# Kernel tuning notes

Hardware: AMD Instinct MI355X
Metric: run time of the kernel (lower is better)

The kernel has to match this reference:

```python
import jax, jax.numpy as jnp
import numpy as np

LN_EPS = 1e-5

def _ln(x, g, b):
    # LayerNorm over last dim; torch normalized_shape=[1,H] on [B,1,H] reduces to this
    mu = jnp.mean(x, axis=-1, keepdims=True)
    var = jnp.var(x, axis=-1, keepdims=True)
    return (x - mu) * jax.lax.rsqrt(var + LN_EPS) * g + b


def setup_inputs() -> dict:
    key = jax.random.key(0)
    B, T, D, H = 32, 2048, 512, 128
    ks = jax.random.split(key, 10)
    stdu = 1.0 / np.sqrt(H)
    u = lambda k, sh: jax.random.uniform(k, sh, jnp.float32, -stdu, stdu)
    return {
        "x": jax.random.normal(ks[0], (B, T, D), jnp.float32),
        "W_f": u(ks[1], (D, H)), "W_i": u(ks[2], (D, H)),
        "W_o": u(ks[3], (D, H)), "W_c": u(ks[4], (D, H)),
        "U_f": u(ks[5], (H, H)), "U_i": u(ks[6], (H, H)),
        "U_o": u(ks[7], (H, H)), "U_c": u(ks[8], (H, H)),
        "b_f": jnp.ones((H,), jnp.float32),
        "b_i": jnp.zeros((H,), jnp.float32),
        "b_o": jnp.zeros((H,), jnp.float32),
        "b_c": jnp.zeros((H,), jnp.float32),
        "ln_f_g": jnp.ones((H,), jnp.float32), "ln_f_b": jnp.zeros((H,), jnp.float32),
        "ln_i_g": jnp.ones((H,), jnp.float32), "ln_i_b": jnp.zeros((H,), jnp.float32),
        "ln_o_g": jnp.ones((H,), jnp.float32), "ln_o_b": jnp.zeros((H,), jnp.float32),
        "ln_c_g": jnp.ones((H,), jnp.float32), "ln_c_b": jnp.zeros((H,), jnp.float32),
        "h0": jnp.zeros((B, H), jnp.float32),
        "c0": jnp.zeros((B, H), jnp.float32),
        "zoneout_mask": jax.random.randint(ks[9], (T,), 0, 2, jnp.int32),
    }


def reference(x, W_f, W_i, W_o, W_c, U_f, U_i, U_o, U_c,
              b_f, b_i, b_o, b_c,
              ln_f_g, ln_f_b, ln_i_g, ln_i_b, ln_o_g, ln_o_b, ln_c_g, ln_c_b,
              h0, c0, zoneout_mask):
    xs = jnp.swapaxes(x, 0, 1)                       # [T, B, D]
    m = zoneout_mask.astype(x.dtype)[:, None, None]  # [T, 1, 1] zoneout indicator

    def step(carry, inp):
        h, c = carry
        x_t, mt = inp
        f = jax.nn.sigmoid(_ln(x_t @ W_f + h @ U_f + b_f, ln_f_g, ln_f_b))
        i = jax.nn.sigmoid(_ln(x_t @ W_i + h @ U_i + b_i, ln_i_g, ln_i_b))
        o = jax.nn.sigmoid(_ln(x_t @ W_o + h @ U_o + b_o, ln_o_g, ln_o_b))
        ch = jax.nn.sigmoid(_ln(x_t @ W_c + h @ U_c + b_c, ln_c_g, ln_c_b))
        c_new = mt * c + (1.0 - mt) * (f * c + i * ch)
        # NOTE: source applies sigmoid (not tanh) to the cell state
        h_new = mt * h + (1.0 - mt) * (o * jax.nn.sigmoid(c_new))
        return (h_new, c_new), h_new

    (h_T, c_T), out_seq = jax.lax.scan(step, (h0, c0), (xs, m))
    return jnp.swapaxes(out_seq, 0, 1), h_T          # [B, T, H], [B, H]
```

## Files before the change

### kernel.cpp

```cpp
#include <hip/hip_runtime.h>
#include <hip/hip_bf16.h>

#define Bx 32
#define Tt 2048
#define Dd 512
#define Hh 128

typedef __attribute__((ext_vector_type(8))) short short8;
typedef __attribute__((ext_vector_type(4))) float f32x4;

static __device__ __forceinline__ short f2bf(float f) {
    __hip_bfloat16 h = __float2bfloat16(f);
    return *reinterpret_cast<short*>(&h);
}
static __device__ __forceinline__ float sigm(float x) {
    return 1.f / (1.f + __expf(-x));
}

template<int CTRL>
static __device__ __forceinline__ float dpp_add(float v) {
    return v + __int_as_float(__builtin_amdgcn_update_dpp(
        0, __float_as_int(v), CTRL, 0xF, 0xF, true));
}
static __device__ __forceinline__ float swz_xor16_add(float v) {
    return v + __int_as_float(__builtin_amdgcn_ds_swizzle(__float_as_int(v), 0x401F));
}

#define BARRIER_LGKM() asm volatile("s_waitcnt lgkmcnt(0)\n\ts_barrier" ::: "memory")

__global__ __launch_bounds__(512, 2) void gemm_xw_mfma(
    const float* __restrict__ X,
    const float* __restrict__ W0, const float* __restrict__ W1,
    const float* __restrict__ W2, const float* __restrict__ W3,
    float* __restrict__ G)
{
    __shared__ __align__(16) short As[128][40];
    __shared__ __align__(16) short Bs[512][40];

    const int tid  = threadIdx.x;
    const int m0   = blockIdx.x * 128;
    const int lane = tid & 63;
    const int w    = tid >> 6;
    const int wr   = w >> 2, wc = w & 3;
    const int l15  = lane & 15, kb = lane >> 4;

    const int bn   = tid;
    const int gate = bn >> 7;
    const int j    = bn & 127;
    const float* __restrict__ Wg = (gate == 0) ? W0 : (gate == 1) ? W1 : (gate == 2) ? W2 : W3;

    const int am = tid >> 2;
    const int ak = (tid & 3) * 8;

    f32x4 acc[4][8];
    #pragma unroll
    for (int mt = 0; mt < 4; ++mt)
        #pragma unroll
        for (int nt = 0; nt < 8; ++nt)
            acc[mt][nt] = (f32x4){0.f, 0.f, 0.f, 0.f};

    for (int k0 = 0; k0 < Dd; k0 += 32) {
        {
            const float4* xp = (const float4*)&X[(size_t)(m0 + am) * Dd + k0 + ak];
            float4 v0 = xp[0], v1 = xp[1];
            short8 s;
            s[0] = f2bf(v0.x); s[1] = f2bf(v0.y); s[2] = f2bf(v0.z); s[3] = f2bf(v0.w);
            s[4] = f2bf(v1.x); s[5] = f2bf(v1.y); s[6] = f2bf(v1.z); s[7] = f2bf(v1.w);
            *(short8*)&As[am][ak] = s;
        }
        #pragma unroll
        for (int rc = 0; rc < 4; ++rc) {
            float v[8];
            #pragma unroll
            for (int r = 0; r < 8; ++r)
                v[r] = Wg[(size_t)(k0 + rc * 8 + r) * Hh + j];
            short8 s;
            #pragma unroll
            for (int r = 0; r < 8; ++r) s[r] = f2bf(v[r]);
            *(short8*)&Bs[bn][rc * 8] = s;
        }
        __syncthreads();

        short8 a[4], b[8];
        #pragma unroll
        for (int mt = 0; mt < 4; ++mt)
            a[mt] = *(const short8*)&As[wr * 64 + mt * 16 + l15][kb * 8];
        #pragma unroll
        for (int nt = 0; nt < 8; ++nt)
            b[nt] = *(const short8*)&Bs[wc * 128 + nt * 16 + l15][kb * 8];
        #pragma unroll
        for (int mt = 0; mt < 4; ++mt)
            #pragma unroll
            for (int nt = 0; nt < 8; ++nt)
                acc[mt][nt] = __builtin_amdgcn_mfma_f32_16x16x32_bf16(a[mt], b[nt], acc[mt][nt], 0, 0, 0);
        __syncthreads();
    }

    #pragma unroll
    for (int mt = 0; mt < 4; ++mt)
        #pragma unroll
        for (int nt = 0; nt < 8; ++nt)
            #pragma unroll
            for (int r = 0; r < 4; ++r)
                G[(size_t)(m0 + wr * 64 + mt * 16 + kb * 4 + r) * 512 + wc * 128 + nt * 16 + l15]
                    = acc[mt][nt][r];
}

__global__ __launch_bounds__(512, 1) void lstm_scan_mfma(
    const float* __restrict__ G,
    const float* __restrict__ Uf, const float* __restrict__ Ui,
    const float* __restrict__ Uo, const float* __restrict__ Uc,
    const float* __restrict__ bf_, const float* __restrict__ bi_,
    const float* __restrict__ bo_, const float* __restrict__ bc_,
    const float* __restrict__ lnfg, const float* __restrict__ lnfb,
    const float* __restrict__ lnig, const float* __restrict__ lnib,
    const float* __restrict__ lnog, const float* __restrict__ lnob,
    const float* __restrict__ lncg, const float* __restrict__ lncb,
    const float* __restrict__ h0, const float* __restrict__ c0,
    const int* __restrict__ zmask,
    float* __restrict__ out, float* __restrict__ hT)
{
    const int tid  = threadIdx.x;
    const int lane = tid & 63;
    const int w    = tid >> 6;
    const int b0   = blockIdx.x * 4;

    __shared__ __align__(16) short Ap[16 * 136];
    __shared__ __align__(16) float ST[512 * 10];
    __shared__ unsigned short act[Tt];
    __shared__ int wsum[8], wpre[8];
    __shared__ int nact_sh;

    const int gate = w >> 1;
    const float* __restrict__ Ug = (gate == 0) ? Uf : (gate == 1) ? Ui : (gate == 2) ? Uo : Uc;
    const int n0  = w * 64;
    const int l15 = lane & 15;
    const int kb  = lane >> 4;

    short8 bfr[4][4];
    #pragma unroll
    for (int nt = 0; nt < 4; ++nt) {
        const int jloc = (n0 & 127) + nt * 16 + l15;
        #pragma unroll
        for (int ks = 0; ks < 4; ++ks) {
            short8 v;
            #pragma unroll
            for (int r = 0; r < 8; ++r) {
                const int krow = ks * 32 + kb * 8 + r;
                v[r] = f2bf(Ug[krow * Hh + jloc]);
            }
            bfr[nt][ks] = v;
        }
    }

    const int rowL = tid >> 5;
    const int bL   = rowL >> 2;
    const int gL   = rowL & 3;
    const int cl   = tid & 31;
    const float* lnGp = (gL == 0) ? lnfg : (gL == 1) ? lnig : (gL == 2) ? lnog : lncg;
    const float* lnBp = (gL == 0) ? lnfb : (gL == 1) ? lnib : (gL == 2) ? lnob : lncb;
    const float* bgp  = (gL == 0) ? bf_  : (gL == 1) ? bi_  : (gL == 2) ? bo_  : bc_;
    float lgam[4], lbet[4], lbias[4];
    #pragma unroll
    for (int kk = 0; kk < 4; ++kk) {
        const int jc = cl + 32 * kk;
        lgam[kk] = lnGp[jc]; lbet[kk] = lnBp[jc]; lbias[kk] = bgp[jc];
    }

    const int ob = tid >> 7;
    const int oj = tid & 127;
    float hval = h0[(b0 + ob) * Hh + oj];
    float cval = c0[(b0 + ob) * Hh + oj];

    for (int i = tid; i < 16 * 136; i += 512) Ap[i] = 0;
    int* zst = (int*)ST;
    for (int t = tid; t < Tt; t += 512) zst[t] = zmask[t];
    __syncthreads();

    Ap[ob * 136 + oj] = f2bf(hval);

    {
        const int base_t = tid * 4;
        const int f0 = (zst[base_t] == 0), f1 = (zst[base_t + 1] == 0);
        const int f2 = (zst[base_t + 2] == 0), f3 = (zst[base_t + 3] == 0);
        const int cnt = f0 + f1 + f2 + f3;
        int scan = cnt;
        #pragma unroll
        for (int off = 1; off <= 32; off <<= 1) {
            int v = __shfl_up(scan, off);
            if (lane >= off) scan += v;
        }
        if (lane == 63) wsum[w] = scan;
        __syncthreads();
        if (tid == 0) {
            int s = 0;
            #pragma unroll
            for (int i = 0; i < 8; ++i) { wpre[i] = s; s += wsum[i]; }
            nact_sh = s;
        }
        __syncthreads();
        int pos = wpre[w] + scan - cnt;
        if (f0) act[pos++] = (unsigned short)(base_t);
        if (f1) act[pos++] = (unsigned short)(base_t + 1);
        if (f2) act[pos++] = (unsigned short)(base_t + 2);
        if (f3) act[pos++] = (unsigned short)(base_t + 3);
    }
    __syncthreads();
    const int nact = nact_sh;

    const int firstA = (nact > 0) ? (int)act[0] : Tt;
    for (int tt = 0; tt < firstA; ++tt)
        out[((size_t)(b0 + ob) * Tt + tt) * Hh + oj] = hval;

    const float* __restrict__ Gbase = G;

#define PREFETCH_G(tq, DST)                                                       \
    do {                                                                          \
        const int _t = (tq);                                                      \
        DST##0[0] = Gbase[((size_t)(b0 + 0) * Tt + _t) * 512 + n0 +  0 + l15];    \
        DST##0[1] = Gbase[((size_t)(b0 + 1) * Tt + _t) * 512 + n0 +  0 + l15];    \
        DST##0[2] = Gbase[((size_t)(b0 + 2) * Tt + _t) * 512 + n0 +  0 + l15];    \
        DST##0[3] = Gbase[((size_t)(b0 + 3) * Tt + _t) * 512 + n0 +  0 + l15];    \
        DST##1[0] = Gbase[((size_t)(b0 + 0) * Tt + _t) * 512 + n0 + 16 + l15];    \
        DST##1[1] = Gbase[((size_t)(b0 + 1) * Tt + _t) * 512 + n0 + 16 + l15];    \
        DST##1[2] = Gbase[((size_t)(b0 + 2) * Tt + _t) * 512 + n0 + 16 + l15];    \
        DST##1[3] = Gbase[((size_t)(b0 + 3) * Tt + _t) * 512 + n0 + 16 + l15];    \
        DST##2[0] = Gbase[((size_t)(b0 + 0) * Tt + _t) * 512 + n0 + 32 + l15];    \
        DST##2[1] = Gbase[((size_t)(b0 + 1) * Tt + _t) * 512 + n0 + 32 + l15];    \
        DST##2[2] = Gbase[((size_t)(b0 + 2) * Tt + _t) * 512 + n0 + 32 + l15];    \
        DST##2[3] = Gbase[((size_t)(b0 + 3) * Tt + _t) * 512 + n0 + 32 + l15];    \
        DST##3[0] = Gbase[((size_t)(b0 + 0) * Tt + _t) * 512 + n0 + 48 + l15];    \
        DST##3[1] = Gbase[((size_t)(b0 + 1) * Tt + _t) * 512 + n0 + 48 + l15];    \
        DST##3[2] = Gbase[((size_t)(b0 + 2) * Tt + _t) * 512 + n0 + 48 + l15];    \
        DST##3[3] = Gbase[((size_t)(b0 + 3) * Tt + _t) * 512 + n0 + 48 + l15];    \
    } while (0)

    f32x4 gA0, gA1, gA2, gA3, gB0, gB1, gB2, gB3;
    if (nact > 0) PREFETCH_G((int)act[0], gA);
    if (nact > 1) PREFETCH_G((int)act[1], gB);

#define LSTM_STEP(KK, CUR)                                                        \
    do {                                                                          \
        const int _k  = (KK);                                                     \
        const int t   = (int)act[_k];                                             \
        const int t2  = (_k + 1 < nact) ? (int)act[_k + 1] : Tt;                  \
        short8 a0 = *(const short8*)&Ap[l15 * 136 +  0 + kb * 8];                 \
        short8 a1 = *(const short8*)&Ap[l15 * 136 + 32 + kb * 8];                 \
        short8 a2 = *(const short8*)&Ap[l15 * 136 + 64 + kb * 8];                 \
        short8 a3 = *(const short8*)&Ap[l15 * 136 + 96 + kb * 8];                 \
        f32x4 C0 = CUR##0, C1 = CUR##1, C2_ = CUR##2, C3 = CUR##3;                \
        f32x4 D0 = {0,0,0,0}, D1 = {0,0,0,0}, D2 = {0,0,0,0}, D3 = {0,0,0,0};     \
        C0  = __builtin_amdgcn_mfma_f32_16x16x32_bf16(a0, bfr[0][0], C0,  0,0,0); \
        C1  = __builtin_amdgcn_mfma_f32_16x16x32_bf16(a0, bfr[1][0], C1,  0,0,0); \
        C2_ = __builtin_amdgcn_mfma_f32_16x16x32_bf16(a0, bfr[2][0], C2_, 0,0,0); \
        C3  = __builtin_amdgcn_mfma_f32_16x16x32_bf16(a0, bfr[3][0], C3,  0,0,0); \
        D0  = __builtin_amdgcn_mfma_f32_16x16x32_bf16(a2, bfr[0][2], D0,  0,0,0); \
        D1  = __builtin_amdgcn_mfma_f32_16x16x32_bf16(a2, bfr[1][2], D1,  0,0,0); \
        D2  = __builtin_amdgcn_mfma_f32_16x16x32_bf16(a2, bfr[2][2], D2,  0,0,0); \
        D3  = __builtin_amdgcn_mfma_f32_16x16x32_bf16(a2, bfr[3][2], D3,  0,0,0); \
        C0  = __builtin_amdgcn_mfma_f32_16x16x32_bf16(a1, bfr[0][1], C0,  0,0,0); \
        C1  = __builtin_amdgcn_mfma_f32_16x16x32_bf16(a1, bfr[1][1], C1,  0,0,0); \
        C2_ = __builtin_amdgcn_mfma_f32_16x16x32_bf16(a1, bfr[2][1], C2_, 0,0,0); \
        C3  = __builtin_amdgcn_mfma_f32_16x16x32_bf16(a1, bfr[3][1], C3,  0,0,0); \
        D0  = __builtin_amdgcn_mfma_f32_16x16x32_bf16(a3, bfr[0][3], D0,  0,0,0); \
        D1  = __builtin_amdgcn_mfma_f32_16x16x32_bf16(a3, bfr[1][3], D1,  0,0,0); \
        D2  = __builtin_amdgcn_mfma_f32_16x16x32_bf16(a3, bfr[2][3], D2,  0,0,0); \
        D3  = __builtin_amdgcn_mfma_f32_16x16x32_bf16(a3, bfr[3][3], D3,  0,0,0); \
        if (_k + 2 < nact) PREFETCH_G((int)act[_k + 2], CUR);                     \
        if (lane < 16) {                                                          \
            *(float2*)&ST[(n0 +  0 + l15) * 10]     = make_float2(C0[0]+D0[0], C0[1]+D0[1]); \
            *(float2*)&ST[(n0 +  0 + l15) * 10 + 2] = make_float2(C0[2]+D0[2], C0[3]+D0[3]); \
            *(float2*)&ST[(n0 + 16 + l15) * 10]     = make_float2(C1[0]+D1[0], C1[1]+D1[1]); \
            *(float2*)&ST[(n0 + 16 + l15) * 10 + 2] = make_float2(C1[2]+D1[2], C1[3]+D1[3]); \
            *(float2*)&ST[(n0 + 32 + l15) * 10]     = make_float2(C2_[0]+D2[0], C2_[1]+D2[1]); \
            *(float2*)&ST[(n0 + 32 + l15) * 10 + 2] = make_float2(C2_[2]+D2[2], C2_[3]+D2[3]); \
            *(float2*)&ST[(n0 + 48 + l15) * 10]     = make_float2(C3[0]+D3[0], C3[1]+D3[1]); \
            *(float2*)&ST[(n0 + 48 + l15) * 10 + 2] = make_float2(C3[2]+D3[2], C3[3]+D3[3]); \
        }                                                                         \
        BARRIER_LGKM();                                                           \
        float s0_ = ST[(gL * 128 + cl +  0) * 10 + bL] + lbias[0];                \
        float s1_ = ST[(gL * 128 + cl + 32) * 10 + bL] + lbias[1];                \
        float s2_ = ST[(gL * 128 + cl + 64) * 10 + bL] + lbias[2];                \
        float s3_ = ST[(gL * 128 + cl + 96) * 10 + bL] + lbias[3];                \
        float sm = (s0_ + s1_) + (s2_ + s3_);                                     \
        float sq = s0_*s0_ + s1_*s1_ + s2_*s2_ + s3_*s3_;                         \
        sm = dpp_add<0xB1>(sm);  sq = dpp_add<0xB1>(sq);                          \
        sm = dpp_add<0x4E>(sm);  sq = dpp_add<0x4E>(sq);                          \
        sm = dpp_add<0x124>(sm); sq = dpp_add<0x124>(sq);                         \
        sm = dpp_add<0x128>(sm); sq = dpp_add<0x128>(sq);                         \
        sm = swz_xor16_add(sm);  sq = swz_xor16_add(sq);                          \
        const float mu   = sm * (1.f / 128.f);                                    \
        const float rstd = rsqrtf(sq * (1.f / 128.f) - mu * mu + 1e-5f);          \
        ST[(gL * 128 + cl +  0) * 10 + bL] = sigm((s0_ - mu) * rstd * lgam[0] + lbet[0]); \
        ST[(gL * 128 + cl + 32) * 10 + bL] = sigm((s1_ - mu) * rstd * lgam[1] + lbet[1]); \
        ST[(gL * 128 + cl + 64) * 10 + bL] = sigm((s2_ - mu) * rstd * lgam[2] + lbet[2]); \
        ST[(gL * 128 + cl + 96) * 10 + bL] = sigm((s3_ - mu) * rstd * lgam[3] + lbet[3]); \
        BARRIER_LGKM();                                                           \
        const float gf  = ST[(0   + oj) * 10 + ob];                               \
        const float gi  = ST[(128 + oj) * 10 + ob];                               \
        const float go  = ST[(256 + oj) * 10 + ob];                               \
        const float gch = ST[(384 + oj) * 10 + ob];                               \
        cval = gf * cval + gi * gch;                                              \
        hval = go * sigm(cval);                                                   \
        Ap[ob * 136 + oj] = f2bf(hval);                                           \
        for (int tt = t; tt < t2; ++tt)                                           \
            out[((size_t)(b0 + ob) * Tt + tt) * Hh + oj] = hval;                  \
        BARRIER_LGKM();                                                           \
    } while (0)

    for (int k = 0; k < nact; k += 2) {
        LSTM_STEP(k, gA);
        if (k + 1 < nact) LSTM_STEP(k + 1, gB);
    }

    hT[(b0 + ob) * Hh + oj] = hval;
#undef LSTM_STEP
#undef PREFETCH_G
}

extern "C" void kernel_launch(void* const* d_in, const int* in_sizes, int n_in,
                              void* d_out, int out_size, void* d_ws, size_t ws_size,
                              hipStream_t stream)
{
    const float* x   = (const float*)d_in[0];
    const float* W_f = (const float*)d_in[1];
    const float* W_i = (const float*)d_in[2];
    const float* W_o = (const float*)d_in[3];
    const float* W_c = (const float*)d_in[4];
    const float* U_f = (const float*)d_in[5];
    const float* U_i = (const float*)d_in[6];
    const float* U_o = (const float*)d_in[7];
    const float* U_c = (const float*)d_in[8];
    const float* b_f = (const float*)d_in[9];
    const float* b_i = (const float*)d_in[10];
    const float* b_o = (const float*)d_in[11];
    const float* b_c = (const float*)d_in[12];
    const float* ln_f_g = (const float*)d_in[13];
    const float* ln_f_b = (const float*)d_in[14];
    const float* ln_i_g = (const float*)d_in[15];
    const float* ln_i_b = (const float*)d_in[16];
    const float* ln_o_g = (const float*)d_in[17];
    const float* ln_o_b = (const float*)d_in[18];
    const float* ln_c_g = (const float*)d_in[19];
    const float* ln_c_b = (const float*)d_in[20];
    const float* h0  = (const float*)d_in[21];
    const float* c0  = (const float*)d_in[22];
    const int*   zm  = (const int*)d_in[23];

    float* out = (float*)d_out;
    float* hT  = out + (size_t)Bx * Tt * Hh;
    float* G   = (float*)d_ws;

    gemm_xw_mfma<<<(Bx * Tt) / 128, 512, 0, stream>>>(x, W_f, W_i, W_o, W_c, G);

    lstm_scan_mfma<<<8, 512, 0, stream>>>(G, U_f, U_i, U_o, U_c,
                                          b_f, b_i, b_o, b_c,
                                          ln_f_g, ln_f_b, ln_i_g, ln_i_b,
                                          ln_o_g, ln_o_b, ln_c_g, ln_c_b,
                                          h0, c0, zm, out, hT);
}
```

Baseline: 1.620 ms.

## Remap LSTM scan so each wave owns all four gates of its columns

```diff
diff --git a/kernel.cpp b/kernel.cpp
--- a/kernel.cpp
+++ b/kernel.cpp
@@ -22,11 +22,16 @@
     return v + __int_as_float(__builtin_amdgcn_update_dpp(
         0, __float_as_int(v), CTRL, 0xF, 0xF, true));
 }
-static __device__ __forceinline__ float swz_xor16_add(float v) {
-    return v + __int_as_float(__builtin_amdgcn_ds_swizzle(__float_as_int(v), 0x401F));
+static __device__ __forceinline__ float rowred16(float v) {
+    v = dpp_add<0xB1>(v);
+    v = dpp_add<0x4E>(v);
+    v = dpp_add<0x124>(v);
+    v = dpp_add<0x128>(v);
+    return v;
 }
 
 #define BARRIER_LGKM() asm volatile("s_waitcnt lgkmcnt(0)\n\ts_barrier" ::: "memory")
+#define WAVE_LDS_FENCE() asm volatile("s_waitcnt lgkmcnt(0)" ::: "memory")
 
 __global__ __launch_bounds__(512, 2) void gemm_xw_mfma(
     const float* __restrict__ X,
@@ -124,65 +129,48 @@
     const int lane = tid & 63;
     const int w    = tid >> 6;
     const int b0   = blockIdx.x * 4;
+    const int l15  = lane & 15;
+    const int kb   = lane >> 4;
+    const int j    = w * 16 + l15;
 
     __shared__ __align__(16) short Ap[16 * 136];
-    __shared__ __align__(16) float ST[512 * 10];
+    __shared__ __align__(16) float SW[8 * 4 * 16 * 4];
+    __shared__ __align__(16) float red[2 * 4 * 8 * 4];
     __shared__ unsigned short act[Tt];
     __shared__ int wsum[8], wpre[8];
     __shared__ int nact_sh;
 
-    const int gate = w >> 1;
-    const float* __restrict__ Ug = (gate == 0) ? Uf : (gate == 1) ? Ui : (gate == 2) ? Uo : Uc;
-    const int n0  = w * 64;
-    const int l15 = lane & 15;
-    const int kb  = lane >> 4;
-
     short8 bfr[4][4];
     #pragma unroll
-    for (int nt = 0; nt < 4; ++nt) {
-        const int jloc = (n0 & 127) + nt * 16 + l15;
+    for (int g = 0; g < 4; ++g) {
+        const float* __restrict__ Ug = (g == 0) ? Uf : (g == 1) ? Ui : (g == 2) ? Uo : Uc;
         #pragma unroll
         for (int ks = 0; ks < 4; ++ks) {
             short8 v;
             #pragma unroll
-            for (int r = 0; r < 8; ++r) {
-                const int krow = ks * 32 + kb * 8 + r;
-                v[r] = f2bf(Ug[krow * Hh + jloc]);
-            }
-            bfr[nt][ks] = v;
+            for (int r = 0; r < 8; ++r)
+                v[r] = f2bf(Ug[(ks * 32 + kb * 8 + r) * Hh + j]);
+            bfr[g][ks] = v;
         }
     }
 
-    const int rowL = tid >> 5;
-    const int bL   = rowL >> 2;
-    const int gL   = rowL & 3;
-    const int cl   = tid & 31;
-    const float* lnGp = (gL == 0) ? lnfg : (gL == 1) ? lnig : (gL == 2) ? lnog : lncg;
-    const float* lnBp = (gL == 0) ? lnfb : (gL == 1) ? lnib : (gL == 2) ? lnob : lncb;
-    const float* bgp  = (gL == 0) ? bf_  : (gL == 1) ? bi_  : (gL == 2) ? bo_  : bc_;
     float lgam[4], lbet[4], lbias[4];
-    #pragma unroll
-    for (int kk = 0; kk < 4; ++kk) {
-        const int jc = cl + 32 * kk;
-        lgam[kk] = lnGp[jc]; lbet[kk] = lnBp[jc]; lbias[kk] = bgp[jc];
-    }
-
-    const int ob = tid >> 7;
-    const int oj = tid & 127;
-    float hval = h0[(b0 + ob) * Hh + oj];
-    float cval = c0[(b0 + ob) * Hh + oj];
+    lgam[0] = lnfg[j]; lbet[0] = lnfb[j]; lbias[0] = bf_[j];
+    lgam[1] = lnig[j]; lbet[1] = lnib[j]; lbias[1] = bi_[j];
+    lgam[2] = lnog[j]; lbet[2] = lnob[j]; lbias[2] = bo_[j];
+    lgam[3] = lncg[j]; lbet[3] = lncb[j]; lbias[3] = bc_[j];
+
+    float hval = h0[(b0 + kb) * Hh + j];
+    float cval = c0[(b0 + kb) * Hh + j];
 
     for (int i = tid; i < 16 * 136; i += 512) Ap[i] = 0;
-    int* zst = (int*)ST;
-    for (int t = tid; t < Tt; t += 512) zst[t] = zmask[t];
     __syncthreads();
-
-    Ap[ob * 136 + oj] = f2bf(hval);
+    Ap[kb * 136 + j] = f2bf(hval);
 
     {
         const int base_t = tid * 4;
-        const int f0 = (zst[base_t] == 0), f1 = (zst[base_t + 1] == 0);
-        const int f2 = (zst[base_t + 2] == 0), f3 = (zst[base_t + 3] == 0);
+        const int f0 = (zmask[base_t] == 0), f1 = (zmask[base_t + 1] == 0);
+        const int f2 = (zmask[base_t + 2] == 0), f3 = (zmask[base_t + 3] == 0);
         const int cnt = f0 + f1 + f2 + f3;
         int scan = cnt;
         #pragma unroll
@@ -210,102 +198,106 @@
 
     const int firstA = (nact > 0) ? (int)act[0] : Tt;
     for (int tt = 0; tt < firstA; ++tt)
-        out[((size_t)(b0 + ob) * Tt + tt) * Hh + oj] = hval;
-
-    const float* __restrict__ Gbase = G;
-
-#define PREFETCH_G(tq, DST)                                                       \
-    do {                                                                          \
-        const int _t = (tq);                                                      \
-        DST##0[0] = Gbase[((size_t)(b0 + 0) * Tt + _t) * 512 + n0 +  0 + l15];    \
-        DST##0[1] = Gbase[((size_t)(b0 + 1) * Tt + _t) * 512 + n0 +  0 + l15];    \
-        DST##0[2] = Gbase[((size_t)(b0 + 2) * Tt + _t) * 512 + n0 +  0 + l15];    \
-        DST##0[3] = Gbase[((size_t)(b0 + 3) * Tt + _t) * 512 + n0 +  0 + l15];    \
-        DST##1[0] = Gbase[((size_t)(b0 + 0) * Tt + _t) * 512 + n0 + 16 + l15];    \
-        DST##1[1] = Gbase[((size_t)(b0 + 1) * Tt + _t) * 512 + n0 + 16 + l15];    \
-        DST##1[2] = Gbase[((size_t)(b0 + 2) * Tt + _t) * 512 + n0 + 16 + l15];    \
-        DST##1[3] = Gbase[((size_t)(b0 + 3) * Tt + _t) * 512 + n0 + 16 + l15];    \
-        DST##2[0] = Gbase[((size_t)(b0 + 0) * Tt + _t) * 512 + n0 + 32 + l15];    \
-        DST##2[1] = Gbase[((size_t)(b0 + 1) * Tt + _t) * 512 + n0 + 32 + l15];    \
-        DST##2[2] = Gbase[((size_t)(b0 + 2) * Tt + _t) * 512 + n0 + 32 + l15];    \
-        DST##2[3] = Gbase[((size_t)(b0 + 3) * Tt + _t) * 512 + n0 + 32 + l15];    \
-        DST##3[0] = Gbase[((size_t)(b0 + 0) * Tt + _t) * 512 + n0 + 48 + l15];    \
-        DST##3[1] = Gbase[((size_t)(b0 + 1) * Tt + _t) * 512 + n0 + 48 + l15];    \
-        DST##3[2] = Gbase[((size_t)(b0 + 2) * Tt + _t) * 512 + n0 + 48 + l15];    \
-        DST##3[3] = Gbase[((size_t)(b0 + 3) * Tt + _t) * 512 + n0 + 48 + l15];    \
+        out[((size_t)(b0 + kb) * Tt + tt) * Hh + j] = hval;
+
+#define PREFETCH_G(tq, DST)                                                     \
+    do {                                                                        \
+        const int _t = (tq);                                                    \
+        DST##0[0] = G[((size_t)(b0 + 0) * Tt + _t) * 512 +   0 + j];            \
+        DST##0[1] = G[((size_t)(b0 + 1) * Tt + _t) * 512 +   0 + j];            \
+        DST##0[2] = G[((size_t)(b0 + 2) * Tt + _t) * 512 +   0 + j];            \
+        DST##0[3] = G[((size_t)(b0 + 3) * Tt + _t) * 512 +   0 + j];            \
+        DST##1[0] = G[((size_t)(b0 + 0) * Tt + _t) * 512 + 128 + j];            \
+        DST##1[1] = G[((size_t)(b0 + 1) * Tt + _t) * 512 + 128 + j];            \
+        DST##1[2] = G[((size_t)(b0 + 2) * Tt + _t) * 512 + 128 + j];            \
+        DST##1[3] = G[((size_t)(b0 + 3) * Tt + _t) * 512 + 128 + j];            \
+        DST##2[0] = G[((size_t)(b0 + 0) * Tt + _t) * 512 + 256 + j];            \
+        DST##2[1] = G[((size_t)(b0 + 1) * Tt + _t) * 512 + 256 + j];            \
+        DST##2[2] = G[((size_t)(b0 + 2) * Tt + _t) * 512 + 256 + j];            \
+        DST##2[3] = G[((size_t)(b0 + 3) * Tt + _t) * 512 + 256 + j];            \
+        DST##3[0] = G[((size_t)(b0 + 0) * Tt + _t) * 512 + 384 + j];            \
+        DST##3[1] = G[((size_t)(b0 + 1) * Tt + _t) * 512 + 384 + j];            \
+        DST##3[2] = G[((size_t)(b0 + 2) * Tt + _t) * 512 + 384 + j];            \
+        DST##3[3] = G[((size_t)(b0 + 3) * Tt + _t) * 512 + 384 + j];            \
     } while (0)
 
     f32x4 gA0, gA1, gA2, gA3, gB0, gB1, gB2, gB3;
     if (nact > 0) PREFETCH_G((int)act[0], gA);
     if (nact > 1) PREFETCH_G((int)act[1], gB);
 
-#define LSTM_STEP(KK, CUR)                                                        \
-    do {                                                                          \
-        const int _k  = (KK);                                                     \
-        const int t   = (int)act[_k];                                             \
-        const int t2  = (_k + 1 < nact) ? (int)act[_k + 1] : Tt;                  \
-        short8 a0 = *(const short8*)&Ap[l15 * 136 +  0 + kb * 8];                 \
-        short8 a1 = *(const short8*)&Ap[l15 * 136 + 32 + kb * 8];                 \
-        short8 a2 = *(const short8*)&Ap[l15 * 136 + 64 + kb * 8];                 \
-        short8 a3 = *(const short8*)&Ap[l15 * 136 + 96 + kb * 8];                 \
-        f32x4 C0 = CUR##0, C1 = CUR##1, C2_ = CUR##2, C3 = CUR##3;                \
-        f32x4 D0 = {0,0,0,0}, D1 = {0,0,0,0}, D2 = {0,0,0,0}, D3 = {0,0,0,0};     \
-        C0  = __builtin_amdgcn_mfma_f32_16x16x32_bf16(a0, bfr[0][0], C0,  0,0,0); \
-        C1  = __builtin_amdgcn_mfma_f32_16x16x32_bf16(a0, bfr[1][0], C1,  0,0,0); \
-        C2_ = __builtin_amdgcn_mfma_f32_16x16x32_bf16(a0, bfr[2][0], C2_, 0,0,0); \
-        C3  = __builtin_amdgcn_mfma_f32_16x16x32_bf16(a0, bfr[3][0], C3,  0,0,0); \
-        D0  = __builtin_amdgcn_mfma_f32_16x16x32_bf16(a2, bfr[0][2], D0,  0,0,0); \
-        D1  = __builtin_amdgcn_mfma_f32_16x16x32_bf16(a2, bfr[1][2], D1,  0,0,0); \
-        D2  = __builtin_amdgcn_mfma_f32_16x16x32_bf16(a2, bfr[2][2], D2,  0,0,0); \
-        D3  = __builtin_amdgcn_mfma_f32_16x16x32_bf16(a2, bfr[3][2], D3,  0,0,0); \
-        C0  = __builtin_amdgcn_mfma_f32_16x16x32_bf16(a1, bfr[0][1], C0,  0,0,0); \
-        C1  = __builtin_amdgcn_mfma_f32_16x16x32_bf16(a1, bfr[1][1], C1,  0,0,0); \
-        C2_ = __builtin_amdgcn_mfma_f32_16x16x32_bf16(a1, bfr[2][1], C2_, 0,0,0); \
-        C3  = __builtin_amdgcn_mfma_f32_16x16x32_bf16(a1, bfr[3][1], C3,  0,0,0); \
-        D0  = __builtin_amdgcn_mfma_f32_16x16x32_bf16(a3, bfr[0][3], D0,  0,0,0); \
-        D1  = __builtin_amdgcn_mfma_f32_16x16x32_bf16(a3, bfr[1][3], D1,  0,0,0); \
-        D2  = __builtin_amdgcn_mfma_f32_16x16x32_bf16(a3, bfr[2][3], D2,  0,0,0); \
-        D3  = __builtin_amdgcn_mfma_f32_16x16x32_bf16(a3, bfr[3][3], D3,  0,0,0); \
-        if (_k + 2 < nact) PREFETCH_G((int)act[_k + 2], CUR);                     \
-        if (lane < 16) {                                                          \
-            *(float2*)&ST[(n0 +  0 + l15) * 10]     = make_float2(C0[0]+D0[0], C0[1]+D0[1]); \
-            *(float2*)&ST[(n0 +  0 + l15) * 10 + 2] = make_float2(C0[2]+D0[2], C0[3]+D0[3]); \
-            *(float2*)&ST[(n0 + 16 + l15) * 10]     = make_float2(C1[0]+D1[0], C1[1]+D1[1]); \
-            *(float2*)&ST[(n0 + 16 + l15) * 10 + 2] = make_float2(C1[2]+D1[2], C1[3]+D1[3]); \
-            *(float2*)&ST[(n0 + 32 + l15) * 10]     = make_float2(C2_[0]+D2[0], C2_[1]+D2[1]); \
-            *(float2*)&ST[(n0 + 32 + l15) * 10 + 2] = make_float2(C2_[2]+D2[2], C2_[3]+D2[3]); \
-            *(float2*)&ST[(n0 + 48 + l15) * 10]     = make_float2(C3[0]+D3[0], C3[1]+D3[1]); \
-            *(float2*)&ST[(n0 + 48 + l15) * 10 + 2] = make_float2(C3[2]+D3[2], C3[3]+D3[3]); \
-        }                                                                         \
-        BARRIER_LGKM();                                                           \
-        float s0_ = ST[(gL * 128 + cl +  0) * 10 + bL] + lbias[0];                \
-        float s1_ = ST[(gL * 128 + cl + 32) * 10 + bL] + lbias[1];                \
-        float s2_ = ST[(gL * 128 + cl + 64) * 10 + bL] + lbias[2];                \
-        float s3_ = ST[(gL * 128 + cl + 96) * 10 + bL] + lbias[3];                \
-        float sm = (s0_ + s1_) + (s2_ + s3_);                                     \
-        float sq = s0_*s0_ + s1_*s1_ + s2_*s2_ + s3_*s3_;                         \
-        sm = dpp_add<0xB1>(sm);  sq = dpp_add<0xB1>(sq);                          \
-        sm = dpp_add<0x4E>(sm);  sq = dpp_add<0x4E>(sq);                          \
-        sm = dpp_add<0x124>(sm); sq = dpp_add<0x124>(sq);                         \
-        sm = dpp_add<0x128>(sm); sq = dpp_add<0x128>(sq);                         \
-        sm = swz_xor16_add(sm);  sq = swz_xor16_add(sq);                          \
-        const float mu   = sm * (1.f / 128.f);                                    \
-        const float rstd = rsqrtf(sq * (1.f / 128.f) - mu * mu + 1e-5f);          \
-        ST[(gL * 128 + cl +  0) * 10 + bL] = sigm((s0_ - mu) * rstd * lgam[0] + lbet[0]); \
-        ST[(gL * 128 + cl + 32) * 10 + bL] = sigm((s1_ - mu) * rstd * lgam[1] + lbet[1]); \
-        ST[(gL * 128 + cl + 64) * 10 + bL] = sigm((s2_ - mu) * rstd * lgam[2] + lbet[2]); \
-        ST[(gL * 128 + cl + 96) * 10 + bL] = sigm((s3_ - mu) * rstd * lgam[3] + lbet[3]); \
-        BARRIER_LGKM();                                                           \
-        const float gf  = ST[(0   + oj) * 10 + ob];                               \
-        const float gi  = ST[(128 + oj) * 10 + ob];                               \
-        const float go  = ST[(256 + oj) * 10 + ob];                               \
-        const float gch = ST[(384 + oj) * 10 + ob];                               \
-        cval = gf * cval + gi * gch;                                              \
-        hval = go * sigm(cval);                                                   \
-        Ap[ob * 136 + oj] = f2bf(hval);                                           \
-        for (int tt = t; tt < t2; ++tt)                                           \
-            out[((size_t)(b0 + ob) * Tt + tt) * Hh + oj] = hval;                  \
-        BARRIER_LGKM();                                                           \
+#define LSTM_STEP(KK, CUR)                                                      \
+    do {                                                                        \
+        const int _k  = (KK);                                                   \
+        const int _t  = (int)act[_k];                                           \
+        const int _t2 = (_k + 1 < nact) ? (int)act[_k + 1] : Tt;                \
+                 \
+        short8 _a0 = *(const short8*)&Ap[l15 * 136 +  0 + kb * 8];              \
+        short8 _a1 = *(const short8*)&Ap[l15 * 136 + 32 + kb * 8];              \
+        short8 _a2 = *(const short8*)&Ap[l15 * 136 + 64 + kb * 8];              \
+        short8 _a3 = *(const short8*)&Ap[l15 * 136 + 96 + kb * 8];              \
+        f32x4 _C0 = CUR##0, _C1 = CUR##1, _C2 = CUR##2, _C3 = CUR##3;           \
+        _C0 = __builtin_amdgcn_mfma_f32_16x16x32_bf16(_a0, bfr[0][0], _C0, 0,0,0); \
+        _C1 = __builtin_amdgcn_mfma_f32_16x16x32_bf16(_a0, bfr[1][0], _C1, 0,0,0); \
+        _C2 = __builtin_amdgcn_mfma_f32_16x16x32_bf16(_a0, bfr[2][0], _C2, 0,0,0); \
+        _C3 = __builtin_amdgcn_mfma_f32_16x16x32_bf16(_a0, bfr[3][0], _C3, 0,0,0); \
+        _C0 = __builtin_amdgcn_mfma_f32_16x16x32_bf16(_a1, bfr[0][1], _C0, 0,0,0); \
+        _C1 = __builtin_amdgcn_mfma_f32_16x16x32_bf16(_a1, bfr[1][1], _C1, 0,0,0); \
+        _C2 = __builtin_amdgcn_mfma_f32_16x16x32_bf16(_a1, bfr[2][1], _C2, 0,0,0); \
+        _C3 = __builtin_amdgcn_mfma_f32_16x16x32_bf16(_a1, bfr[3][1], _C3, 0,0,0); \
+        _C0 = __builtin_amdgcn_mfma_f32_16x16x32_bf16(_a2, bfr[0][2], _C0, 0,0,0); \
+        _C1 = __builtin_amdgcn_mfma_f32_16x16x32_bf16(_a2, bfr[1][2], _C1, 0,0,0); \
+        _C2 = __builtin_amdgcn_mfma_f32_16x16x32_bf16(_a2, bfr[2][2], _C2, 0,0,0); \
+        _C3 = __builtin_amdgcn_mfma_f32_16x16x32_bf16(_a2, bfr[3][2], _C3, 0,0,0); \
+        _C0 = __builtin_amdgcn_mfma_f32_16x16x32_bf16(_a3, bfr[0][3], _C0, 0,0,0); \
+        _C1 = __builtin_amdgcn_mfma_f32_16x16x32_bf16(_a3, bfr[1][3], _C1, 0,0,0); \
+        _C2 = __builtin_amdgcn_mfma_f32_16x16x32_bf16(_a3, bfr[2][3], _C2, 0,0,0); \
+        _C3 = __builtin_amdgcn_mfma_f32_16x16x32_bf16(_a3, bfr[3][3], _C3, 0,0,0); \
+        if (_k + 2 < nact) PREFETCH_G((int)act[_k + 2], CUR);                   \
+        \
+        if (lane < 16) {                                                        \
+            *(float4*)&SW[w * 256 +   0 + l15 * 4] = make_float4(_C0[0], _C0[1], _C0[2], _C0[3]); \
+            *(float4*)&SW[w * 256 +  64 + l15 * 4] = make_float4(_C1[0], _C1[1], _C1[2], _C1[3]); \
+            *(float4*)&SW[w * 256 + 128 + l15 * 4] = make_float4(_C2[0], _C2[1], _C2[2], _C2[3]); \
+            *(float4*)&SW[w * 256 + 192 + l15 * 4] = make_float4(_C3[0], _C3[1], _C3[2], _C3[3]); \
+        }                                                                       \
+        WAVE_LDS_FENCE();                                                       \
+                  \
+        float _s[4], _sm[4], _sq[4];                                            \
+        _s[0] = SW[w * 256 +   0 + l15 * 4 + kb] + lbias[0];                    \
+        _s[1] = SW[w * 256 +  64 + l15 * 4 + kb] + lbias[1];                    \
+        _s[2] = SW[w * 256 + 128 + l15 * 4 + kb] + lbias[2];                    \
+        _s[3] = SW[w * 256 + 192 + l15 * 4 + kb] + lbias[3];                    \
+        _Pragma("unroll")                                                       \
+        for (int _g = 0; _g < 4; ++_g) {                                        \
+            _sm[_g] = rowred16(_s[_g]);                                         \
+            _sq[_g] = rowred16(_s[_g] * _s[_g]);                                \
+        }                                                                       \
+        if (l15 == 0) {                                                         \
+            *(float4*)&red[(0 * 4 + kb) * 32 + w * 4] = make_float4(_sm[0], _sm[1], _sm[2], _sm[3]); \
+            *(float4*)&red[(1 * 4 + kb) * 32 + w * 4] = make_float4(_sq[0], _sq[1], _sq[2], _sq[3]); \
+        }                                                                       \
+        BARRIER_LGKM();                                                         \
+         \
+        f32x4 _ps = *(const f32x4*)&red[(0 * 4 + kb) * 32 + (l15 & 7) * 4];     \
+        f32x4 _pq = *(const f32x4*)&red[(1 * 4 + kb) * 32 + (l15 & 7) * 4];     \
+        _Pragma("unroll")                                                       \
+        for (int _g = 0; _g < 4; ++_g) {                                        \
+            _ps[_g] = rowred16(_ps[_g]);                                        \
+            _pq[_g] = rowred16(_pq[_g]);                                        \
+        }                                                                       \
+        float _v[4];                                                            \
+        _Pragma("unroll")                                                       \
+        for (int _g = 0; _g < 4; ++_g) {                                        \
+            const float _mu   = _ps[_g] * (1.f / 256.f);   \
+            const float _rstd = rsqrtf(_pq[_g] * (1.f / 256.f) - _mu * _mu + 1e-5f); \
+            _v[_g] = sigm((_s[_g] - _mu) * _rstd * lgam[_g] + lbet[_g]);        \
+        }                                                                       \
+        cval = _v[0] * cval + _v[1] * _v[3];                                    \
+        hval = _v[2] * sigm(cval);                   \
+        Ap[kb * 136 + j] = f2bf(hval);                                          \
+        for (int _tt = _t; _tt < _t2; ++_tt)                                    \
+            out[((size_t)(b0 + kb) * Tt + _tt) * Hh + j] = hval;                \
+        BARRIER_LGKM();                                                         \
     } while (0)
 
     for (int k = 0; k < nact; k += 2) {
@@ -313,7 +305,7 @@
         if (k + 1 < nact) LSTM_STEP(k + 1, gB);
     }
 
-    hT[(b0 + ob) * Hh + oj] = hval;
+    hT[(b0 + kb) * Hh + j] = hval;
 #undef LSTM_STEP
 #undef PREFETCH_G
 }
```

New measurement: 1.958 ms. 20.9% more time.
